# Optimization experiments

Hardware: AMD Instinct MI355X
Metric: run time of the kernel (lower is better)

## Reference

```python
import jax, jax.numpy as jnp
import numpy as np

B, C, Hf, Wf = 32, 512, 16, 16
S = Hf * Wf            # 256 kv tokens
D = 2048               # d_model
DIN = 512              # d_input (attention embed dim)
HEADS = 8
DH = DIN // HEADS
T = 50                 # iterations (internal ticks)
M = 25                 # memory_length
HH = 16                # memory_hidden_dims
NSA = 512              # n_synch_action
NSO = 512              # n_synch_out
OUT = 1000             # out_dims


def _ln(x, g, b, eps=1e-5):
    mu = x.mean(-1, keepdims=True)
    var = ((x - mu) ** 2).mean(-1, keepdims=True)
    return (x - mu) / jnp.sqrt(var + eps) * g + b


def _glu(x):
    a, b = jnp.split(x, 2, axis=-1)
    return a * jax.nn.sigmoid(b)


def setup_inputs() -> dict:
    key = jax.random.key(0)
    ki = iter(jax.random.split(key, 40))
    def rn(shape, s=0.02):
        return jax.random.normal(next(ki), shape, jnp.float32) * s
    inp = {}
    inp['x'] = jax.random.normal(next(ki), (B, C, Hf, Wf), jnp.float32)
    # kv_proj: Linear(C->DIN) + LayerNorm
    inp['kv_w'] = rn((C, DIN)); inp['kv_b'] = jnp.zeros((DIN,), jnp.float32)
    inp['ln_kv_g'] = jnp.ones((DIN,), jnp.float32); inp['ln_kv_b'] = jnp.zeros((DIN,), jnp.float32)
    # q_proj: Linear(NSA->DIN)
    inp['q_w'] = rn((NSA, DIN)); inp['q_b'] = jnp.zeros((DIN,), jnp.float32)
    # MultiheadAttention projections
    inp['Wq'] = rn((DIN, DIN)); inp['bq'] = jnp.zeros((DIN,), jnp.float32)
    inp['Wk'] = rn((DIN, DIN)); inp['bk'] = jnp.zeros((DIN,), jnp.float32)
    inp['Wv'] = rn((DIN, DIN)); inp['bv'] = jnp.zeros((DIN,), jnp.float32)
    inp['Wo'] = rn((DIN, DIN)); inp['bo'] = jnp.zeros((DIN,), jnp.float32)
    # synapse: Linear(DIN+D -> 2D) + GLU + LayerNorm(D)
    inp['syn_w'] = rn((DIN + D, 2 * D)); inp['syn_b'] = jnp.zeros((2 * D,), jnp.float32)
    inp['ln_syn_g'] = jnp.ones((D,), jnp.float32); inp['ln_syn_b'] = jnp.zeros((D,), jnp.float32)
    # per-neuron NLMs (SuperLinear weights: (in,out,N))
    inp['nlm_w1'] = rn((M, 2 * HH, D), 0.1); inp['nlm_b1'] = jnp.zeros((1, D, 2 * HH), jnp.float32)
    inp['nlm_w2'] = rn((HH, 2, D), 0.1); inp['nlm_b2'] = jnp.zeros((1, D, 2), jnp.float32)
    # output projector
    inp['out_w'] = rn((NSO, OUT)); inp['out_b'] = jnp.zeros((OUT,), jnp.float32)
    # learnable decay params (clamped to [0,15] in forward)
    inp['decay_action'] = jax.random.uniform(next(ki), (NSA,), jnp.float32)
    inp['decay_out'] = jax.random.uniform(next(ki), (NSO,), jnp.float32)
    # learned start state
    inp['start_trace'] = rn((D, M), 0.05)
    inp['start_act'] = rn((D,), 0.05)
    # random-pairing neuron indices (fixed at init in the original)
    inp['idx_la'] = jax.random.randint(next(ki), (NSA,), 0, D)
    inp['idx_ra'] = jax.random.randint(next(ki), (NSA,), 0, D)
    inp['idx_lo'] = jax.random.randint(next(ki), (NSO,), 0, D)
    inp['idx_ro'] = jax.random.randint(next(ki), (NSO,), 0, D)
    return inp


def reference(x, kv_w, kv_b, ln_kv_g, ln_kv_b, q_w, q_b, Wq, bq, Wk, bk, Wv, bv, Wo, bo,
              syn_w, syn_b, ln_syn_g, ln_syn_b, nlm_w1, nlm_b1, nlm_w2, nlm_b2,
              out_w, out_b, decay_action, decay_out, start_trace, start_act,
              idx_la, idx_ra, idx_lo, idx_ro):
    # featurise: identity backbone, flatten spatial to tokens, project to DIN
    feats = x.reshape(B, C, S).transpose(0, 2, 1)                 # (B,S,C)
    kv = _ln(feats @ kv_w + kv_b, ln_kv_g, ln_kv_b)               # (B,S,DIN)
    kh = (kv @ Wk + bk).reshape(B, S, HEADS, DH).transpose(0, 2, 1, 3)  # (B,H,S,DH)
    vh = (kv @ Wv + bv).reshape(B, S, HEADS, DH).transpose(0, 2, 1, 3)
    r_a = jnp.exp(-jnp.clip(decay_action, 0.0, 15.0))[None]       # (1,NSA)
    r_o = jnp.exp(-jnp.clip(decay_out, 0.0, 15.0))[None]          # (1,NSO)

    def nlm(trace):  # per-neuron MLP over the memory axis: (B,D,M) -> (B,D)
        h = _glu(jnp.einsum('bdm,mhd->bdh', trace, nlm_w1) + nlm_b1)
        return _glu(jnp.einsum('bdh,hod->bdo', h, nlm_w2) + nlm_b2)[..., 0]

    act0 = jnp.broadcast_to(start_act[None], (B, D))
    trace0 = jnp.broadcast_to(start_trace[None], (B, D, M))
    # out-synchronisation initialised from the start state (before the loop)
    a_o0 = act0[:, idx_lo] * act0[:, idx_ro]
    b_o0 = jnp.ones_like(a_o0)
    a_a0 = jnp.zeros((B, NSA), jnp.float32)
    b_a0 = jnp.zeros((B, NSA), jnp.float32)
    log_out = jnp.log(jnp.float32(OUT))
    scale = 1.0 / jnp.sqrt(jnp.float32(DH))

    def step(carry, _):
        trace, act, a_a, b_a, a_o, b_o = carry
        # action synchronisation (decayed pairwise products, sync = alpha/sqrt(beta))
        a_a = r_a * a_a + act[:, idx_la] * act[:, idx_ra]
        b_a = r_a * b_a + 1.0
        sync_a = a_a / jnp.sqrt(b_a)
        # attention readout (single query token)
        q = sync_a @ q_w + q_b                                    # (B,DIN)
        qh = (q @ Wq + bq).reshape(B, HEADS, 1, DH)
        attn = jax.nn.softmax(jnp.einsum('bhqd,bhkd->bhqk', qh, kh) * scale, -1)
        o = jnp.einsum('bhqk,bhkd->bhqd', attn, vh).transpose(0, 2, 1, 3).reshape(B, DIN)
        attn_out = o @ Wo + bo
        # synapse MLP -> new pre-activation state
        pre = jnp.concatenate([attn_out, act], axis=-1)           # (B,DIN+D)
        state = _ln(_glu(pre @ syn_w + syn_b), ln_syn_g, ln_syn_b)
        trace = jnp.concatenate([trace[:, :, 1:], state[:, :, None]], axis=-1)
        act = nlm(trace)                                          # (B,D)
        # output synchronisation + prediction
        a_o = r_o * a_o + act[:, idx_lo] * act[:, idx_ro]
        b_o = r_o * b_o + 1.0
        sync_o = a_o / jnp.sqrt(b_o)
        pred = sync_o @ out_w + out_b                             # (B,OUT)
        logp = jax.nn.log_softmax(pred, -1)
        ne = -(jnp.exp(logp) * logp).sum(-1) / log_out
        cert = jnp.stack([ne, 1.0 - ne], axis=-1)                 # (B,2)
        return (trace, act, a_a, b_a, a_o, b_o), (pred, cert, sync_o)

    _, (preds, certs, syncs) = jax.lax.scan(step, (trace0, act0, a_a0, b_a0, a_o0, b_o0), None, length=T)
    predictions = jnp.transpose(preds, (1, 2, 0))                 # (B,OUT,T)
    certainties = jnp.transpose(certs, (1, 2, 0))                 # (B,2,T)
    return predictions, certainties, syncs[-1]
```

## Files before the change

kernel.cpp:

```cpp
#include <hip/hip_runtime.h>
#include <math.h>

#define BB 32
#define CC 512
#define SS 256
#define DD 2048
#define DIN 512
#define NH 8
#define DHD 64
#define TT 50
#define MM 25
#define HHID 16
#define NSA 512
#define NSO 512
#define NOUT 1000

__device__ __forceinline__ unsigned short f2bf(float f) {
    unsigned u = __float_as_uint(f);
    u += 0x7fffu + ((u >> 16) & 1u);
    return (unsigned short)(u >> 16);
}
__device__ __forceinline__ float bf2f(unsigned short s) {
    return __uint_as_float((unsigned)s << 16);
}
__device__ __forceinline__ float blo(unsigned u) {
    return __uint_as_float(u << 16);
}
__device__ __forceinline__ float bhi(unsigned u) {
    return __uint_as_float(u & 0xffff0000u);
}

__global__ void init_kernel(const float* __restrict__ dec_a, const float* __restrict__ dec_o,
                            const float* __restrict__ start_act, const float* __restrict__ start_trace,
                            const int* __restrict__ idx_lo, const int* __restrict__ idx_ro,
                            float* __restrict__ r_a, float* __restrict__ r_o,
                            float* __restrict__ a_a, float* __restrict__ b_a,
                            float* __restrict__ a_o, float* __restrict__ b_o,
                            float* __restrict__ trace)
{
    int i = blockIdx.x * 256 + threadIdx.x;
    if (i < 512) {
        r_a[i] = expf(-fminf(fmaxf(dec_a[i], 0.f), 15.f));
        r_o[i] = expf(-fminf(fmaxf(dec_o[i], 0.f), 15.f));
    }
    if (i < BB * NSA) {
        a_a[i] = 0.f; b_a[i] = 0.f;
        int j = i & 511;
        a_o[i] = start_act[idx_lo[j]] * start_act[idx_ro[j]];
        b_o[i] = 1.f;
    }
    if (i < BB * MM * DD) {
        int rem = i % (MM * DD);
        int m = rem / DD, d = rem % DD;
        trace[i] = start_trace[d * MM + m];
    }
}

template<int AMODE, int SMODE>
__global__ void gemm64(const float* __restrict__ A, const float* __restrict__ Bm,
                       const float* __restrict__ bias, float* __restrict__ Cm,
                       int Mdim, int Ndim, int Kdim)
{
    __shared__ float As[16 * 65];
    __shared__ float Bs[16 * 64];
    int row0 = blockIdx.x * 64;
    int col0 = blockIdx.y * 64;
    int t = threadIdx.x;
    int tx = t & 15, ty = t >> 4;
    float acc[4][4] = {};
    for (int k0 = 0; k0 < Kdim; k0 += 16) {
        if (AMODE == 0) {
            for (int i = t; i < 1024; i += 256) {
                int kk = i & 15, r = i >> 4;
                As[kk * 65 + r] = A[(size_t)(row0 + r) * Kdim + k0 + kk];
            }
        } else {
            int b = row0 / SS, s0 = row0 % SS;
            for (int i = t; i < 1024; i += 256) {
                int r = i & 63, kk = i >> 6;
                As[kk * 65 + r] = A[((size_t)b * CC + k0 + kk) * SS + s0 + r];
            }
        }
        for (int i = t; i < 1024; i += 256) {
            int c = i & 63, kk = i >> 6;
            Bs[kk * 64 + c] = Bm[(size_t)(k0 + kk) * Ndim + col0 + c];
        }
        __syncthreads();
        #pragma unroll
        for (int kk = 0; kk < 16; ++kk) {
            float a[4], bb[4];
            #pragma unroll
            for (int i = 0; i < 4; i++) a[i] = As[kk * 65 + ty * 4 + i];
            #pragma unroll
            for (int j = 0; j < 4; j++) bb[j] = Bs[kk * 64 + tx * 4 + j];
            #pragma unroll
            for (int i = 0; i < 4; i++)
                #pragma unroll
                for (int j = 0; j < 4; j++) acc[i][j] += a[i] * bb[j];
        }
        __syncthreads();
    }
    #pragma unroll
    for (int i = 0; i < 4; i++)
        #pragma unroll
        for (int j = 0; j < 4; j++) {
            int row = row0 + ty * 4 + i, col = col0 + tx * 4 + j;
            float v = acc[i][j] + (bias ? bias[col] : 0.f);
            if (SMODE == 0) {
                Cm[(size_t)row * Ndim + col] = v;
            } else if (SMODE == 1) {
                int b = row / SS, s = row % SS, h = col >> 6, dh = col & 63;
                Cm[(((size_t)b * NH + h) * DHD + dh) * SS + s] = v;
            } else {
                int b = row / SS, s = row % SS, h = col >> 6, dh = col & 63;
                Cm[(((size_t)b * NH + h) * SS + s) * DHD + dh] = v;
            }
        }
}

__global__ void ln_rows(float* __restrict__ buf, const float* __restrict__ g,
                        const float* __restrict__ bta)
{
    int row = blockIdx.x, t = threadIdx.x;
    __shared__ float red[256];
    float v0 = buf[(size_t)row * 512 + t];
    float v1 = buf[(size_t)row * 512 + 256 + t];
    red[t] = v0 + v1; __syncthreads();
    for (int off = 128; off; off >>= 1) { if (t < off) red[t] += red[t + off]; __syncthreads(); }
    float mu = red[0] * (1.f / 512.f); __syncthreads();
    float d0 = v0 - mu, d1 = v1 - mu;
    red[t] = d0 * d0 + d1 * d1; __syncthreads();
    for (int off = 128; off; off >>= 1) { if (t < off) red[t] += red[t + off]; __syncthreads(); }
    float rstd = 1.f / sqrtf(red[0] * (1.f / 512.f) + 1e-5f);
    buf[(size_t)row * 512 + t]       = d0 * rstd * g[t] + bta[t];
    buf[(size_t)row * 512 + 256 + t] = d1 * rstd * g[t + 256] + bta[t + 256];
}

__global__ void bqq_kernel(const float* __restrict__ q_b, const float* __restrict__ Wq,
                           const float* __restrict__ bq, float* __restrict__ bqq)
{
    int c = blockIdx.x * 256 + threadIdx.x;
    if (c >= 512) return;
    float acc = bq[c];
    for (int k = 0; k < 512; k++) acc += q_b[k] * Wq[k * 512 + c];
    bqq[c] = acc;
}

__global__ void bias2_kernel(const float* __restrict__ bo, const float* __restrict__ syn_w,
                             const float* __restrict__ syn_b, float* __restrict__ bias2)
{
    int c = blockIdx.x * 256 + threadIdx.x;
    if (c >= 4096) return;
    float acc = syn_b[c];
    for (int k = 0; k < 512; k++) acc += bo[k] * syn_w[(size_t)k * 4096 + c];
    bias2[c] = acc;
}

__global__ void wt_build(const float* __restrict__ W2, const float* __restrict__ syn_w,
                         unsigned short* __restrict__ WTh)
{
    __shared__ float tile[32][33];
    int k0 = blockIdx.x * 32, c0 = blockIdx.y * 32;
    int t = threadIdx.x;
    int col = t & 31, rq = t >> 5;
    #pragma unroll
    for (int q = 0; q < 4; ++q) {
        int kk = q * 8 + rq;
        int k = k0 + kk;
        const float* src = (k < 512 ? W2 : syn_w) + (size_t)k * 4096 + c0;
        tile[kk][col] = src[col];
    }
    __syncthreads();
    #pragma unroll
    for (int q = 0; q < 4; ++q) {
        int cc = q * 8 + rq;
        WTh[(size_t)(c0 + cc) * 2560 + k0 + col] = f2bf(tile[col][cc]);
    }
}

__global__ void conv_kernel(const float* __restrict__ khT, const float* __restrict__ vh,
                            const float* __restrict__ w1,
                            unsigned short* __restrict__ khTh, unsigned short* __restrict__ vhh,
                            unsigned short* __restrict__ w1h)
{
    int i = blockIdx.x * 256 + threadIdx.x;
    khTh[i] = f2bf(khT[i]);
    vhh[i]  = f2bf(vh[i]);
    if (i < 25 * 32 * DD) w1h[i] = f2bf(w1[i]);
}

__global__ void act0_kernel(const float* __restrict__ start_act, float* __restrict__ act0slot)
{
    int i = blockIdx.x * 256 + threadIdx.x;
    if (i < BB * DD) act0slot[i] = start_act[i & (DD - 1)];
}

__global__ void pad_outw(const float* __restrict__ out_w, const float* __restrict__ out_b,
                         float* __restrict__ out_wp, float* __restrict__ out_bp)
{
    int i = blockIdx.x * 256 + threadIdx.x;
    if (i < 512 * 1024) {
        int r = i >> 10, c = i & 1023;
        out_wp[i] = (c < 1000) ? out_w[r * 1000 + c] : 0.f;
    }
    if (i < 1024) out_bp[i] = (i < 1000) ? out_b[i] : 0.f;
}

__global__ __launch_bounds__(256) void k1_front(
    const float* __restrict__ act, const int* __restrict__ la, const int* __restrict__ ra,
    const float* __restrict__ r_a,
    const float* __restrict__ aold, const float* __restrict__ bold,
    float* __restrict__ anew, float* __restrict__ bnew,
    const float* __restrict__ Wqq, const float* __restrict__ bqq,
    const unsigned short* __restrict__ khTh, const unsigned short* __restrict__ vhh,
    float* __restrict__ obuf)
{
    __shared__ float sa[512];
    __shared__ float qp[256];
    __shared__ float qs[64];
    __shared__ float ps[256];
    __shared__ float red[256];
    int bh = blockIdx.x, b = bh >> 3, h = bh & 7;
    int tid = threadIdx.x;
    const float* actb = act + b * DD;
    for (int j = tid; j < 512; j += 256) {
        float p = actb[la[j]] * actb[ra[j]];
        float r = r_a[j];
        float aa = r * aold[b * 512 + j] + p;
        float bb = r * bold[b * 512 + j] + 1.f;
        sa[j] = aa / sqrtf(bb);
        if (h == 0) { anew[b * 512 + j] = aa; bnew[b * 512 + j] = bb; }
    }
    __syncthreads();
    {
        int cl = tid & 63, q = tid >> 6;
        const float* wcol = Wqq + h * 64 + cl;
        float acc = 0.f;
        #pragma unroll 8
        for (int k = q * 128; k < q * 128 + 128; ++k)
            acc += sa[k] * wcol[k * 512];
        qp[tid] = acc;
    }
    __syncthreads();
    if (tid < 64)
        qs[tid] = qp[tid] + qp[tid + 64] + qp[tid + 128] + qp[tid + 192] + bqq[h * 64 + tid];
    __syncthreads();
    const unsigned short* kb = khTh + (size_t)bh * 64 * 256;
    float sc = 0.f;
    #pragma unroll 8
    for (int dh = 0; dh < 64; ++dh) sc += qs[dh] * bf2f(kb[dh * 256 + tid]);
    sc *= 0.125f;
    red[tid] = sc; __syncthreads();
    for (int off = 128; off; off >>= 1) { if (tid < off) red[tid] = fmaxf(red[tid], red[tid + off]); __syncthreads(); }
    float mx = red[0]; __syncthreads();
    float e = expf(sc - mx);
    red[tid] = e; __syncthreads();
    for (int off = 128; off; off >>= 1) { if (tid < off) red[tid] += red[tid + off]; __syncthreads(); }
    float inv = 1.f / red[0];
    ps[tid] = e * inv;
    __syncthreads();
    int dh = tid & 63, ch = tid >> 6;
    const unsigned short* vb = vhh + (size_t)bh * 256 * 64;
    float acc = 0.f;
    for (int s = ch * 64; s < ch * 64 + 64; ++s) acc += ps[s] * bf2f(vb[s * 64 + dh]);
    red[tid] = acc; __syncthreads();
    if (tid < 128) red[tid] += red[tid + 128];
    __syncthreads();
    if (tid < 64) obuf[b * 512 + h * 64 + tid] = red[tid] + red[tid + 64];
}

__global__ __launch_bounds__(256) void k2_glu(
    const float* __restrict__ obuf, const float* __restrict__ act,
    const unsigned short* __restrict__ WTh, const float* __restrict__ bias2,
    float* __restrict__ glbufT, float* __restrict__ partials)
{
    __shared__ float As[2 * 32 * 160];
    int tid = threadIdx.x, blk = blockIdx.x;
    int kh = tid >> 7;
    int cpair = (tid >> 5) & 3;
    int r = tid & 31;
    int c = blk * 4 + cpair;
    const unsigned short* wta = WTh + (size_t)c * 2560 + kh * 1280;
    const unsigned short* wtb = WTh + (size_t)(c + 2048) * 2560 + kh * 1280;
    float acc_a = 0.f, acc_b = 0.f;
    for (int ri = 0; ri < 8; ++ri) {
        __syncthreads();
        #pragma unroll
        for (int q = 0; q < 10; ++q) {
            int i = tid + q * 256;
            int hh = i / 1280;
            int rem = i - hh * 1280;
            int rr = rem / 40, kg = rem - (rem / 40) * 40;
            int k = hh * 1280 + ri * 160 + kg * 4;
            float4 v;
            if (k < 512) v = *(const float4*)(obuf + rr * 512 + k);
            else         v = *(const float4*)(act + rr * 2048 + (k - 512));
            *(float4*)(As + hh * 5120 + rr * 160 + ((kg ^ (rr & 7)) << 2)) = v;
        }
        __syncthreads();
        const float* Ar = As + kh * 5120 + r * 160;
        const unsigned short* wtaa = wta + ri * 160;
        const unsigned short* wtbb = wtb + ri * 160;
        int sw = r & 7;
        #pragma unroll 4
        for (int kc = 0; kc < 20; ++kc) {
            uint4 wa = *(const uint4*)(wtaa + kc * 8);
            uint4 wb = *(const uint4*)(wtbb + kc * 8);
            float4 a0 = *(const float4*)(Ar + (((2 * kc) ^ sw) << 2));
            float4 a1 = *(const float4*)(Ar + (((2 * kc + 1) ^ sw) << 2));
            acc_a += a0.x * blo(wa.x) + a0.y * bhi(wa.x) + a0.z * blo(wa.y) + a0.w * bhi(wa.y)
                   + a1.x * blo(wa.z) + a1.y * bhi(wa.z) + a1.z * blo(wa.w) + a1.w * bhi(wa.w);
            acc_b += a0.x * blo(wb.x) + a0.y * bhi(wb.x) + a0.z * blo(wb.y) + a0.w * bhi(wb.y)
                   + a1.x * blo(wb.z) + a1.y * bhi(wb.z) + a1.z * blo(wb.w) + a1.w * bhi(wb.w);
        }
    }
    __syncthreads();
    float* red_a = As;
    float* red_b = As + 128;
    float* gls   = As + 256;
    float* gl2s  = As + 384;
    if (kh == 1) {
        red_a[cpair * 32 + r] = acc_a;
        red_b[cpair * 32 + r] = acc_b;
    }
    __syncthreads();
    if (kh == 0) {
        float ua = acc_a + red_a[cpair * 32 + r] + bias2[c];
        float ub = acc_b + red_b[cpair * 32 + r] + bias2[c + 2048];
        float gl = ua * (1.f / (1.f + expf(-ub)));
        glbufT[c * 32 + r] = gl;
        gls[cpair * 32 + r] = gl;
        gl2s[cpair * 32 + r] = gl * gl;
    }
    __syncthreads();
    if (tid < 32) {
        float s = 0.f, s2 = 0.f;
        #pragma unroll
        for (int cp = 0; cp < 4; ++cp) { s += gls[cp * 32 + tid]; s2 += gl2s[cp * 32 + tid]; }
        partials[blk * 64 + tid * 2]     = s;
        partials[blk * 64 + tid * 2 + 1] = s2;
    }
}

#define K4_LDS_FLOATS (12800 + 2176 + 256 + 256 + 16)
__global__ __launch_bounds__(256) void k4_nlm(
    const float* __restrict__ glbufT, const float* __restrict__ partials,
    const float* __restrict__ g, const float* __restrict__ bta,
    float* __restrict__ trace,
    const unsigned short* __restrict__ w1h, const float* __restrict__ b1,
    const float* __restrict__ w2, const float* __restrict__ b2,
    float* __restrict__ actout, int t_iter)
{
    extern __shared__ float lds[];
    float* wlds  = lds;
    float* cross = lds + 12800;
    float* r1 = lds + 14976;
    float* r2 = lds + 15232;
    float* sm = lds + 15488;
    int tid = threadIdx.x, blk = blockIdx.x;
    int dtile = blk & 127, bgrp = blk >> 7;
    int d0 = dtile * 16, b0 = bgrp * 8;
    int hh = tid >> 7;
    int b_l = (tid >> 4) & 7;
    int d_l = tid & 15;
    int b = b0 + b_l, d = d0 + d_l;

    for (int q = 0; q < 50; ++q) {
        int i = tid + q * 256;
        wlds[i] = bf2f(w1h[(size_t)(i >> 4) * 2048 + d0 + (i & 15)]);
    }
    {
        int bb = tid >> 5, j = tid & 31;
        int bstat = b0 + bb;
        float s = 0.f, s2 = 0.f;
        #pragma unroll
        for (int q = 0; q < 16; ++q) {
            int kblk = j + 32 * q;
            s  += partials[kblk * 64 + bstat * 2];
            s2 += partials[kblk * 64 + bstat * 2 + 1];
        }
        r1[tid] = s; r2[tid] = s2;
        __syncthreads();
        for (int off = 16; off; off >>= 1) {
            if (j < off) { r1[tid] += r1[tid + off]; r2[tid] += r2[tid + off]; }
            __syncthreads();
        }
        if (j == 0) {
            float mu = r1[tid] * (1.f / 2048.f);
            float var = r2[tid] * (1.f / 2048.f) - mu * mu;
            sm[bb * 2] = mu;
            sm[bb * 2 + 1] = 1.f / sqrtf(var + 1e-5f);
        }
        __syncthreads();
    }
    float mu = sm[b_l * 2], rstd = sm[b_l * 2 + 1];
    float gl = glbufT[d * 32 + b];
    float nv = (gl - mu) * rstd * g[d] + bta[d];
    int newrow = t_iter % MM;
    if (hh == 0) trace[((size_t)b * MM + newrow) * DD + d] = nv;

    float hp[16];
    {
        const float* b1d = b1 + d * 32 + hh * 16;
        #pragma unroll
        for (int h = 0; h < 16; h++) hp[h] = b1d[h];
    }
    const float* trb = trace + (size_t)b * MM * DD + d;
    for (int m = 0; m < 24; m++) {
        int mph = (t_iter + 1 + m) % 25;
        float tv = trb[(size_t)mph * DD];
        const float* wm = wlds + (m * 32 + hh * 16) * 16 + d_l;
        #pragma unroll
        for (int h = 0; h < 16; h++) hp[h] += tv * wm[h * 16];
    }
    {
        const float* wm = wlds + (24 * 32 + hh * 16) * 16 + d_l;
        #pragma unroll
        for (int h = 0; h < 16; h++) hp[h] += nv * wm[h * 16];
    }
    if (hh == 1) {
        float* cx = cross + (b_l * 16 + d_l) * 17;
        #pragma unroll
        for (int h = 0; h < 16; h++) cx[h] = hp[h];
    }
    __syncthreads();
    if (hh == 0) {
        const float* cx = cross + (b_l * 16 + d_l) * 17;
        float o0 = b2[d * 2], o1 = b2[d * 2 + 1];
        #pragma unroll
        for (int h = 0; h < 16; h++) {
            float hv = hp[h] * (1.f / (1.f + expf(-cx[h])));
            o0 += hv * w2[((size_t)h * 2) * DD + d];
            o1 += hv * w2[((size_t)h * 2 + 1) * DD + d];
        }
        actout[b * DD + d] = o0 * (1.f / (1.f + expf(-o1)));
    }
}

__global__ __launch_bounds__(256) void k_syncscan(
    const float* __restrict__ acthist, const int* __restrict__ lo, const int* __restrict__ ro,
    const float* __restrict__ r_o,
    const float* __restrict__ a_o0, const float* __restrict__ b_o0,
    float* __restrict__ so_hist, float* __restrict__ out_sync)
{
    int idx = blockIdx.x * 256 + threadIdx.x;
    int b = idx >> 9, j = idx & 511;
    float aa = a_o0[idx], bb = b_o0[idx];
    float rr = r_o[j];
    int il = lo[j], ir = ro[j];
    const float* ah = acthist + (size_t)(BB * DD) + b * DD;
    float s = 0.f;
    for (int t = 0; t < TT; ++t) {
        float p = ah[il] * ah[ir];
        aa = rr * aa + p;
        bb = rr * bb + 1.f;
        s = aa / sqrtf(bb);
        so_hist[(size_t)t * (BB * 512) + idx] = s;
        ah += BB * DD;
    }
    out_sync[idx] = s;
}

__global__ __launch_bounds__(256) void k6_cert(
    const float* __restrict__ predt, float* __restrict__ d_out)
{
    int t_iter = blockIdx.x >> 5, b = blockIdx.x & 31, t = threadIdx.x;
    __shared__ float red[256];
    const float* pr = predt + ((size_t)t_iter * 32 + b) * 1024;
    float pv[4];
    float mx = -1e30f;
    #pragma unroll
    for (int ii = 0; ii < 4; ++ii) {
        int c = t + ii * 256;
        float v = -1e30f;
        if (c < 1000) {
            v = pr[c];
            d_out[(size_t)b * NOUT * TT + (size_t)c * TT + t_iter] = v;
        }
        pv[ii] = v;
        mx = fmaxf(mx, v);
    }
    red[t] = mx; __syncthreads();
    for (int off = 128; off; off >>= 1) { if (t < off) red[t] = fmaxf(red[t], red[t + off]); __syncthreads(); }
    mx = red[0]; __syncthreads();
    float s1 = 0.f, s2 = 0.f;
    #pragma unroll
    for (int ii = 0; ii < 4; ++ii) {
        int c = t + ii * 256;
        if (c < 1000) { float xx = pv[ii] - mx; float e = expf(xx); s1 += e; s2 += e * xx; }
    }
    red[t] = s1; __syncthreads();
    for (int off = 128; off; off >>= 1) { if (t < off) red[t] += red[t + off]; __syncthreads(); }
    s1 = red[0]; __syncthreads();
    red[t] = s2; __syncthreads();
    for (int off = 128; off; off >>= 1) { if (t < off) red[t] += red[t + off]; __syncthreads(); }
    s2 = red[0];
    if (t == 0) {
        float ne = -(s2 / s1 - logf(s1)) * (1.f / logf(1000.f));
        size_t base = (size_t)BB * NOUT * TT + (size_t)b * 2 * TT + t_iter;
        d_out[base] = ne;
        d_out[base + TT] = 1.f - ne;
    }
}

extern "C" void kernel_launch(void* const* d_in, const int* in_sizes, int n_in,
                              void* d_out, int out_size, void* d_ws, size_t ws_size,
                              hipStream_t stream)
{
    const float* x        = (const float*)d_in[0];
    const float* kv_w     = (const float*)d_in[1];
    const float* kv_b     = (const float*)d_in[2];
    const float* ln_kv_g  = (const float*)d_in[3];
    const float* ln_kv_b  = (const float*)d_in[4];
    const float* q_w      = (const float*)d_in[5];
    const float* q_b      = (const float*)d_in[6];
    const float* Wq       = (const float*)d_in[7];
    const float* bq       = (const float*)d_in[8];
    const float* Wk       = (const float*)d_in[9];
    const float* bk       = (const float*)d_in[10];
    const float* Wv       = (const float*)d_in[11];
    const float* bv       = (const float*)d_in[12];
    const float* Wo       = (const float*)d_in[13];
    const float* bo       = (const float*)d_in[14];
    const float* syn_w    = (const float*)d_in[15];
    const float* syn_b    = (const float*)d_in[16];
    const float* ln_syn_g = (const float*)d_in[17];
    const float* ln_syn_b = (const float*)d_in[18];
    const float* nlm_w1   = (const float*)d_in[19];
    const float* nlm_b1   = (const float*)d_in[20];
    const float* nlm_w2   = (const float*)d_in[21];
    const float* nlm_b2   = (const float*)d_in[22];
    const float* out_w    = (const float*)d_in[23];
    const float* out_b    = (const float*)d_in[24];
    const float* dec_a    = (const float*)d_in[25];
    const float* dec_o    = (const float*)d_in[26];
    const float* start_tr = (const float*)d_in[27];
    const float* start_ac = (const float*)d_in[28];
    const int*   idx_la   = (const int*)d_in[29];
    const int*   idx_ra   = (const int*)d_in[30];
    const int*   idx_lo   = (const int*)d_in[31];
    const int*   idx_ro   = (const int*)d_in[32];
    float* out = (float*)d_out;

    float* w = (float*)d_ws;
    float* kvbuf = w;            w += (size_t)8192 * 512;
    float* khT   = w;            w += (size_t)8192 * 512;
    float* vhb   = w;            w += (size_t)8192 * 512;
    float* Wqq   = w;            w += (size_t)512 * 512;
    float* bqq   = w;            w += 512;
    float* W2    = w;            w += (size_t)512 * 4096;
    float* bias2 = w;            w += 4096;
    float* r_a   = w;            w += 512;
    float* r_o   = w;            w += 512;
    float* a_a   = w;            w += 2 * BB * NSA;
    float* b_a   = w;            w += 2 * BB * NSA;
    float* a_o   = w;            w += BB * NSO;
    float* b_o   = w;            w += BB * NSO;
    float* trace = w;            w += (size_t)BB * MM * DD;
    float* obuf  = w;            w += BB * DIN;
    float* glbufT = w;           w += (size_t)DD * BB;
    float* partials = w;         w += 512 * 32 * 2;
    unsigned short* WTh  = (unsigned short*)w;  w += (size_t)4096 * 2560 / 2;
    unsigned short* khTh = (unsigned short*)w;  w += (size_t)8192 * 512 / 2;
    unsigned short* vhh  = (unsigned short*)w;  w += (size_t)8192 * 512 / 2;
    unsigned short* w1h  = (unsigned short*)w;  w += (size_t)25 * 32 * DD / 2;

    float* acthist = kvbuf;
    float* so_hist = vhb;
    float* predt   = vhb + 819200;
    float* out_wp  = khT;
    float* out_bp  = khT + 524288;

    init_kernel<<<6400, 256, 0, stream>>>(dec_a, dec_o, start_ac, start_tr, idx_lo, idx_ro,
                                          r_a, r_o, a_a, b_a, a_o, b_o, trace);
    gemm64<1, 0><<<dim3(128, 8), 256, 0, stream>>>(x, kv_w, kv_b, kvbuf, 8192, 512, 512);
    ln_rows<<<8192, 256, 0, stream>>>(kvbuf, ln_kv_g, ln_kv_b);
    gemm64<0, 1><<<dim3(128, 8), 256, 0, stream>>>(kvbuf, Wk, bk, khT, 8192, 512, 512);
    gemm64<0, 2><<<dim3(128, 8), 256, 0, stream>>>(kvbuf, Wv, bv, vhb, 8192, 512, 512);
    gemm64<0, 0><<<dim3(8, 8), 256, 0, stream>>>(q_w, Wq, nullptr, Wqq, 512, 512, 512);
    bqq_kernel<<<2, 256, 0, stream>>>(q_b, Wq, bq, bqq);
    gemm64<0, 0><<<dim3(8, 64), 256, 0, stream>>>(Wo, syn_w, nullptr, W2, 512, 4096, 512);
    bias2_kernel<<<16, 256, 0, stream>>>(bo, syn_w, syn_b, bias2);
    wt_build<<<dim3(80, 128), 256, 0, stream>>>(W2, syn_w, WTh);
    conv_kernel<<<16384, 256, 0, stream>>>(khT, vhb, nlm_w1, khTh, vhh, w1h);
    act0_kernel<<<256, 256, 0, stream>>>(start_ac, acthist);

    float* out_sync = out + (size_t)BB * NOUT * TT + (size_t)BB * 2 * TT;

    static int lds_attr_set = 0;
    if (!lds_attr_set) {
        hipFuncSetAttribute(reinterpret_cast<const void*>(k4_nlm),
                            hipFuncAttributeMaxDynamicSharedMemorySize,
                            K4_LDS_FLOATS * 4);
        lds_attr_set = 1;
    }

    for (int t = 0; t < TT; ++t) {
        int par = t & 1;
        const float* act_t = acthist + (size_t)t * (BB * DD);
        float* act_n = acthist + (size_t)(t + 1) * (BB * DD);
        k1_front<<<256, 256, 0, stream>>>(act_t, idx_la, idx_ra, r_a,
                                          a_a + par * (BB * 512), b_a + par * (BB * 512),
                                          a_a + (par ^ 1) * (BB * 512), b_a + (par ^ 1) * (BB * 512),
                                          Wqq, bqq, khTh, vhh, obuf);
        k2_glu<<<512, 256, 0, stream>>>(obuf, act_t, WTh, bias2, glbufT, partials);
        k4_nlm<<<512, 256, K4_LDS_FLOATS * 4, stream>>>(glbufT, partials,
                                            ln_syn_g, ln_syn_b, trace,
                                            w1h, nlm_b1, nlm_w2, nlm_b2, act_n, t);
    }

    k_syncscan<<<64, 256, 0, stream>>>(acthist, idx_lo, idx_ro, r_o, a_o, b_o,
                                       so_hist, out_sync);
    pad_outw<<<2048, 256, 0, stream>>>(out_w, out_b, out_wp, out_bp);
    gemm64<0, 0><<<dim3(25, 16), 256, 0, stream>>>(so_hist, out_wp, out_bp, predt,
                                                   1600, 1024, 512);
    k6_cert<<<1600, 256, 0, stream>>>(predt, out);
}
```

Measured before the change: 4.405 ms.

## Store NLM trace in bf16, fuse bf16 K/V output into larger-tile GEMM

The rolling memory trace is now held in bf16 rather than fp32, which halves the bytes the per-iteration NLM kernel reads and writes across the 50 ticks. The K/V projection GEMMs write bf16 head-major layouts directly from their epilogue, so the separate fp32-to-bf16 conversion pass and its extra fp32 buffers are no longer needed. A new 128x64-tile GEMM variant is used for the large setup projections to raise per-thread work and data reuse. The trade-off is lower precision in the stored trace history, and more registers per thread in the larger-tile GEMM.

New measurement: 4.247 ms. 1.04x faster.

```diff
diff --git a/kernel.cpp b/kernel.cpp
--- a/kernel.cpp
+++ b/kernel.cpp
@@ -36,7 +36,7 @@
                             float* __restrict__ r_a, float* __restrict__ r_o,
                             float* __restrict__ a_a, float* __restrict__ b_a,
                             float* __restrict__ a_o, float* __restrict__ b_o,
-                            float* __restrict__ trace)
+                            unsigned short* __restrict__ trace)
 {
     int i = blockIdx.x * 256 + threadIdx.x;
     if (i < 512) {
@@ -52,11 +52,10 @@
     if (i < BB * MM * DD) {
         int rem = i % (MM * DD);
         int m = rem / DD, d = rem % DD;
-        trace[i] = start_trace[d * MM + m];
-    }
-}
-
-template<int AMODE, int SMODE>
+        trace[i] = f2bf(start_trace[d * MM + m]);
+    }
+}
+
 __global__ void gemm64(const float* __restrict__ A, const float* __restrict__ Bm,
                        const float* __restrict__ bias, float* __restrict__ Cm,
                        int Mdim, int Ndim, int Kdim)
@@ -69,51 +68,103 @@
     int tx = t & 15, ty = t >> 4;
     float acc[4][4] = {};
     for (int k0 = 0; k0 < Kdim; k0 += 16) {
+        for (int i = t; i < 1024; i += 256) {
+            int kk = i & 15, r = i >> 4;
+            As[kk * 65 + r] = A[(size_t)(row0 + r) * Kdim + k0 + kk];
+        }
+        for (int i = t; i < 1024; i += 256) {
+            int c = i & 63, kk = i >> 6;
+            Bs[kk * 64 + c] = Bm[(size_t)(k0 + kk) * Ndim + col0 + c];
+        }
+        __syncthreads();
+        #pragma unroll
+        for (int kk = 0; kk < 16; ++kk) {
+            float a[4], bb[4];
+            #pragma unroll
+            for (int i = 0; i < 4; i++) a[i] = As[kk * 65 + ty * 4 + i];
+            #pragma unroll
+            for (int j = 0; j < 4; j++) bb[j] = Bs[kk * 64 + tx * 4 + j];
+            #pragma unroll
+            for (int i = 0; i < 4; i++)
+                #pragma unroll
+                for (int j = 0; j < 4; j++) acc[i][j] += a[i] * bb[j];
+        }
+        __syncthreads();
+    }
+    #pragma unroll
+    for (int i = 0; i < 4; i++)
+        #pragma unroll
+        for (int j = 0; j < 4; j++) {
+            int row = row0 + ty * 4 + i, col = col0 + tx * 4 + j;
+            Cm[(size_t)row * Ndim + col] = acc[i][j] + (bias ? bias[col] : 0.f);
+        }
+}
+
+template<int AMODE, int SMODE>
+__global__ __launch_bounds__(256) void gemm128(
+    const float* __restrict__ A, const float* __restrict__ Bm,
+    const float* __restrict__ bias, float* __restrict__ Cm,
+    int Mdim, int Ndim, int Kdim)
+{
+    __shared__ float As[16 * 129];
+    __shared__ float Bs[16 * 64];
+    int row0 = blockIdx.x * 128;
+    int col0 = blockIdx.y * 64;
+    int t = threadIdx.x;
+    int tx = t & 15, ty = t >> 4;
+    float acc[8][4] = {};
+    for (int k0 = 0; k0 < Kdim; k0 += 16) {
         if (AMODE == 0) {
-            for (int i = t; i < 1024; i += 256) {
+            #pragma unroll
+            for (int q = 0; q < 8; ++q) {
+                int i = t + q * 256;
                 int kk = i & 15, r = i >> 4;
-                As[kk * 65 + r] = A[(size_t)(row0 + r) * Kdim + k0 + kk];
+                As[kk * 129 + r] = A[(size_t)(row0 + r) * Kdim + k0 + kk];
             }
         } else {
             int b = row0 / SS, s0 = row0 % SS;
-            for (int i = t; i < 1024; i += 256) {
-                int r = i & 63, kk = i >> 6;
-                As[kk * 65 + r] = A[((size_t)b * CC + k0 + kk) * SS + s0 + r];
+            #pragma unroll
+            for (int q = 0; q < 8; ++q) {
+                int i = t + q * 256;
+                int r = i & 127, kk = i >> 7;
+                As[kk * 129 + r] = A[((size_t)b * CC + k0 + kk) * SS + s0 + r];
             }
         }
-        for (int i = t; i < 1024; i += 256) {
+        #pragma unroll
+        for (int q = 0; q < 4; ++q) {
+            int i = t + q * 256;
             int c = i & 63, kk = i >> 6;
             Bs[kk * 64 + c] = Bm[(size_t)(k0 + kk) * Ndim + col0 + c];
         }
         __syncthreads();
         #pragma unroll
         for (int kk = 0; kk < 16; ++kk) {
-            float a[4], bb[4];
-            #pragma unroll
-            for (int i = 0; i < 4; i++) a[i] = As[kk * 65 + ty * 4 + i];
+            float a[8], bb[4];
+            #pragma unroll
+            for (int i = 0; i < 8; i++) a[i] = As[kk * 129 + ty * 8 + i];
             #pragma unroll
             for (int j = 0; j < 4; j++) bb[j] = Bs[kk * 64 + tx * 4 + j];
             #pragma unroll
-            for (int i = 0; i < 4; i++)
+            for (int i = 0; i < 8; i++)
                 #pragma unroll
                 for (int j = 0; j < 4; j++) acc[i][j] += a[i] * bb[j];
         }
         __syncthreads();
     }
     #pragma unroll
-    for (int i = 0; i < 4; i++)
+    for (int i = 0; i < 8; i++)
         #pragma unroll
         for (int j = 0; j < 4; j++) {
-            int row = row0 + ty * 4 + i, col = col0 + tx * 4 + j;
+            int row = row0 + ty * 8 + i, col = col0 + tx * 4 + j;
             float v = acc[i][j] + (bias ? bias[col] : 0.f);
             if (SMODE == 0) {
                 Cm[(size_t)row * Ndim + col] = v;
-            } else if (SMODE == 1) {
+            } else if (SMODE == 3) {
                 int b = row / SS, s = row % SS, h = col >> 6, dh = col & 63;
-                Cm[(((size_t)b * NH + h) * DHD + dh) * SS + s] = v;
-            } else {
+                ((unsigned short*)Cm)[(((size_t)b * NH + h) * DHD + dh) * SS + s] = f2bf(v);
+            } else if (SMODE == 4) {
                 int b = row / SS, s = row % SS, h = col >> 6, dh = col & 63;
-                Cm[(((size_t)b * NH + h) * SS + s) * DHD + dh] = v;
+                ((unsigned short*)Cm)[(((size_t)b * NH + h) * SS + s) * DHD + dh] = f2bf(v);
             }
         }
 }
@@ -178,14 +229,9 @@
     }
 }
 
-__global__ void conv_kernel(const float* __restrict__ khT, const float* __restrict__ vh,
-                            const float* __restrict__ w1,
-                            unsigned short* __restrict__ khTh, unsigned short* __restrict__ vhh,
-                            unsigned short* __restrict__ w1h)
+__global__ void conv_w1(const float* __restrict__ w1, unsigned short* __restrict__ w1h)
 {
     int i = blockIdx.x * 256 + threadIdx.x;
-    khTh[i] = f2bf(khT[i]);
-    vhh[i]  = f2bf(vh[i]);
     if (i < 25 * 32 * DD) w1h[i] = f2bf(w1[i]);
 }
 
@@ -346,7 +392,7 @@
 __global__ __launch_bounds__(256) void k4_nlm(
     const float* __restrict__ glbufT, const float* __restrict__ partials,
     const float* __restrict__ g, const float* __restrict__ bta,
-    float* __restrict__ trace,
+    unsigned short* __restrict__ trace,
     const unsigned short* __restrict__ w1h, const float* __restrict__ b1,
     const float* __restrict__ w2, const float* __restrict__ b2,
     float* __restrict__ actout, int t_iter)
@@ -397,7 +443,7 @@
     float gl = glbufT[d * 32 + b];
     float nv = (gl - mu) * rstd * g[d] + bta[d];
     int newrow = t_iter % MM;
-    if (hh == 0) trace[((size_t)b * MM + newrow) * DD + d] = nv;
+    if (hh == 0) trace[((size_t)b * MM + newrow) * DD + d] = f2bf(nv);
 
     float hp[16];
     {
@@ -405,10 +451,10 @@
         #pragma unroll
         for (int h = 0; h < 16; h++) hp[h] = b1d[h];
     }
-    const float* trb = trace + (size_t)b * MM * DD + d;
+    const unsigned short* trb = trace + (size_t)b * MM * DD + d;
     for (int m = 0; m < 24; m++) {
         int mph = (t_iter + 1 + m) % 25;
-        float tv = trb[(size_t)mph * DD];
+        float tv = bf2f(trb[(size_t)mph * DD]);
         const float* wm = wlds + (m * 32 + hh * 16) * 16 + d_l;
         #pragma unroll
         for (int h = 0; h < 16; h++) hp[h] += tv * wm[h * 16];
@@ -544,8 +590,8 @@
 
     float* w = (float*)d_ws;
     float* kvbuf = w;            w += (size_t)8192 * 512;
-    float* khT   = w;            w += (size_t)8192 * 512;
-    float* vhb   = w;            w += (size_t)8192 * 512;
+    float* bigA  = w;            w += (size_t)8192 * 512;
+    float* bigB  = w;            w += (size_t)8192 * 512;
     float* Wqq   = w;            w += (size_t)512 * 512;
     float* bqq   = w;            w += 512;
     float* W2    = w;            w += (size_t)512 * 4096;
@@ -556,33 +602,33 @@
     float* b_a   = w;            w += 2 * BB * NSA;
     float* a_o   = w;            w += BB * NSO;
     float* b_o   = w;            w += BB * NSO;
-    float* trace = w;            w += (size_t)BB * MM * DD;
     float* obuf  = w;            w += BB * DIN;
     float* glbufT = w;           w += (size_t)DD * BB;
     float* partials = w;         w += 512 * 32 * 2;
+    unsigned short* trace = (unsigned short*)w;  w += (size_t)BB * MM * DD / 2;
     unsigned short* WTh  = (unsigned short*)w;  w += (size_t)4096 * 2560 / 2;
     unsigned short* khTh = (unsigned short*)w;  w += (size_t)8192 * 512 / 2;
     unsigned short* vhh  = (unsigned short*)w;  w += (size_t)8192 * 512 / 2;
     unsigned short* w1h  = (unsigned short*)w;  w += (size_t)25 * 32 * DD / 2;
 
     float* acthist = kvbuf;
-    float* so_hist = vhb;
-    float* predt   = vhb + 819200;
-    float* out_wp  = khT;
-    float* out_bp  = khT + 524288;
+    float* out_wp  = bigA;
+    float* out_bp  = bigA + 524288;
+    float* so_hist = bigB;
+    float* predt   = bigB + 819200;
 
     init_kernel<<<6400, 256, 0, stream>>>(dec_a, dec_o, start_ac, start_tr, idx_lo, idx_ro,
                                           r_a, r_o, a_a, b_a, a_o, b_o, trace);
-    gemm64<1, 0><<<dim3(128, 8), 256, 0, stream>>>(x, kv_w, kv_b, kvbuf, 8192, 512, 512);
+    gemm128<1, 0><<<dim3(64, 8), 256, 0, stream>>>(x, kv_w, kv_b, kvbuf, 8192, 512, 512);
     ln_rows<<<8192, 256, 0, stream>>>(kvbuf, ln_kv_g, ln_kv_b);
-    gemm64<0, 1><<<dim3(128, 8), 256, 0, stream>>>(kvbuf, Wk, bk, khT, 8192, 512, 512);
-    gemm64<0, 2><<<dim3(128, 8), 256, 0, stream>>>(kvbuf, Wv, bv, vhb, 8192, 512, 512);
-    gemm64<0, 0><<<dim3(8, 8), 256, 0, stream>>>(q_w, Wq, nullptr, Wqq, 512, 512, 512);
+    gemm128<0, 3><<<dim3(64, 8), 256, 0, stream>>>(kvbuf, Wk, bk, (float*)khTh, 8192, 512, 512);
+    gemm128<0, 4><<<dim3(64, 8), 256, 0, stream>>>(kvbuf, Wv, bv, (float*)vhh, 8192, 512, 512);
+    gemm64<<<dim3(8, 8), 256, 0, stream>>>(q_w, Wq, nullptr, Wqq, 512, 512, 512);
     bqq_kernel<<<2, 256, 0, stream>>>(q_b, Wq, bq, bqq);
-    gemm64<0, 0><<<dim3(8, 64), 256, 0, stream>>>(Wo, syn_w, nullptr, W2, 512, 4096, 512);
+    gemm128<0, 0><<<dim3(4, 64), 256, 0, stream>>>(Wo, syn_w, nullptr, W2, 512, 4096, 512);
     bias2_kernel<<<16, 256, 0, stream>>>(bo, syn_w, syn_b, bias2);
     wt_build<<<dim3(80, 128), 256, 0, stream>>>(W2, syn_w, WTh);
-    conv_kernel<<<16384, 256, 0, stream>>>(khT, vhb, nlm_w1, khTh, vhh, w1h);
+    conv_w1<<<6400, 256, 0, stream>>>(nlm_w1, w1h);
     act0_kernel<<<256, 256, 0, stream>>>(start_ac, acthist);
 
     float* out_sync = out + (size_t)BB * NOUT * TT + (size_t)BB * 2 * TT;
@@ -612,7 +658,7 @@
     k_syncscan<<<64, 256, 0, stream>>>(acthist, idx_lo, idx_ro, r_o, a_o, b_o,
                                        so_hist, out_sync);
     pad_outw<<<2048, 256, 0, stream>>>(out_w, out_b, out_wp, out_bp);
-    gemm64<0, 0><<<dim3(25, 16), 256, 0, stream>>>(so_hist, out_wp, out_bp, predt,
-                                                   1600, 1024, 512);
+    gemm64<<<dim3(25, 16), 256, 0, stream>>>(so_hist, out_wp, out_bp, predt,
+                                             1600, 1024, 512);
     k6_cert<<<1600, 256, 0, stream>>>(predt, out);
 }
```
